# Performance work log

Hardware: AMD Instinct MI355X
Metric: run time of the kernel (lower is better)

The kernel has to match this reference:

```python
import jax, jax.numpy as jnp
import numpy as np

HEADS, DIM_HEAD = 16, 64
MAX_FREQ = 256.0

def axial_freqs(H, W):
    # rotary_embedding_torch, freqs_for='pixel': base freqs = linspace(1, max_freq/2, dim//2)*pi
    # with rotary dim = DIM_HEAD//2 per axis, so DIM_HEAD//4 base frequencies per axis.
    nf = DIM_HEAD // 4
    base = jnp.linspace(1.0, MAX_FREQ / 2.0, nf) * jnp.pi
    def per_axis(n):
        pos = jnp.linspace(-1.0, 1.0, n)              # pixel positions in [-1, 1]
        fr = pos[:, None] * base[None, :]             # (n, DIM_HEAD//4)
        return jnp.repeat(fr, 2, axis=-1)             # (n, DIM_HEAD//2), interleaved repeat
    fh = jnp.broadcast_to(per_axis(H)[:, None, :], (H, W, DIM_HEAD // 2))
    fw = jnp.broadcast_to(per_axis(W)[None, :, :], (H, W, DIM_HEAD // 2))
    return jnp.concatenate([fh, fw], axis=-1)         # (H, W, DIM_HEAD)

def rotate_half(x):
    # interleaved-pair rotation: (x0,x1,x2,x3,...) -> (-x1,x0,-x3,x2,...)
    x2 = x.reshape(x.shape[:-1] + (-1, 2))
    a, b = x2[..., 0], x2[..., 1]
    return jnp.stack([-b, a], axis=-1).reshape(x.shape)

def apply_rot(freqs, t):
    return t * jnp.cos(freqs) + rotate_half(t) * jnp.sin(freqs)

def setup_inputs() -> dict:
    key = jax.random.key(0)
    ks = jax.random.split(key, 6)
    B, T, H, W, dim = 1, 2, 16, 16, 1024
    inner = HEADS * DIM_HEAD
    S, K = H * W, 144
    x = jax.random.normal(ks[0], (B, T, H, W, dim), jnp.float32)
    w_qkv = jax.random.normal(ks[1], (3 * inner, dim), jnp.float32) * (dim ** -0.5)
    w_out = jax.random.normal(ks[2], (dim, inner), jnp.float32) * (inner ** -0.5)
    b_out = jnp.zeros((dim,), jnp.float32)
    out_not_top_k = jax.random.normal(ks[3], (B * T, HEADS, S, DIM_HEAD), jnp.float32) * 0.02
    top_k_indices = jax.random.randint(ks[4], (B * T, HEADS, S, K), 0, S, jnp.int32)
    return {"x": x, "w_qkv": w_qkv, "w_out": w_out, "b_out": b_out,
            "out_not_top_k": out_not_top_k, "top_k_indices": top_k_indices}

def reference(x, w_qkv, w_out, b_out, out_not_top_k, top_k_indices):
    B, T, H, W, dim = x.shape
    inner = HEADS * DIM_HEAD
    S = H * W
    # qkv projection (torch Linear: y = x @ W^T)
    qkv = jnp.einsum('bthwc,oc->bthwo', x, w_qkv)
    q, k, v = jnp.split(qkv, 3, axis=-1)

    def to_grid(t):
        t = t.reshape(B * T, H, W, HEADS, DIM_HEAD)
        return jnp.transpose(t, (0, 3, 1, 2, 4))       # (BT, h, H, W, d)
    q, k, v = map(to_grid, (q, k, v))

    freqs = axial_freqs(H, W)                          # (H, W, d), broadcasts over (BT, h)
    q = apply_rot(freqs, q)
    k = apply_rot(freqs, k)

    q = q.reshape(B * T, HEADS, S, DIM_HEAD)
    k = k.reshape(B * T, HEADS, S, DIM_HEAD)
    v = v.reshape(B * T, HEADS, S, DIM_HEAD)

    scale = DIM_HEAD ** -0.5
    idx = top_k_indices[..., None]                      # (BT, h, S, K, 1)
    # per-query gather of top-k keys/values: out[b,h,s,k,:] = k[b,h,idx[b,h,s,k],:]
    k_g = jnp.take_along_axis(k[:, :, None, :, :], idx, axis=3)  # (BT, h, S, K, d)
    v_g = jnp.take_along_axis(v[:, :, None, :, :], idx, axis=3)

    scores = jnp.einsum('bhsd,bhskd->bhsk', q, k_g) * scale
    probs = jax.nn.softmax(scores, axis=-1)
    out_top = jnp.einsum('bhsk,bhskd->bhsd', probs, v_g)

    out = out_top + out_not_top_k                       # (BT, h, S, d)
    out = jnp.transpose(out.reshape(B * T, HEADS, H, W, DIM_HEAD), (0, 2, 3, 1, 4))
    out = out.reshape(B, T, H, W, inner)
    return jnp.einsum('bthwi,oi->bthwo', out, w_out) + b_out
```

## Files before the change

### kernel.cpp

```cpp
#include <hip/hip_runtime.h>
#include <hip/hip_bf16.h>
#include <math.h>

#define BTN   2
#define NH    16
#define SEQ   256
#define DH    64
#define DIMF  1024
#define KTOP  144
#define QT    32
#define PI_F  3.14159265358979323846f

typedef _Float16 half8 __attribute__((ext_vector_type(8)));
typedef _Float16 half4v __attribute__((ext_vector_type(4)));
typedef float f32x4 __attribute__((ext_vector_type(4)));

#define GLDS(src, dst) __builtin_amdgcn_global_load_lds( \
        (const __attribute__((address_space(1))) void*)(src), \
        (__attribute__((address_space(3))) void*)(dst), 16, 0, 0)

#define N0Q (524288 / 4)
#define N1Q (3145728 / 4)
#define N2Q (1048576 / 4)
__global__ __launch_bounds__(256)
void cvt3_kernel(const float* __restrict__ a, const float* __restrict__ b,
                 const float* __restrict__ c,
                 _Float16* __restrict__ da, _Float16* __restrict__ db,
                 _Float16* __restrict__ dc)
{
    int q = blockIdx.x * 256 + threadIdx.x;
    const float* s; _Float16* d; int off;
    if (q < N0Q)            { s = a; d = da; off = q; }
    else if (q < N0Q + N1Q) { s = b; d = db; off = q - N0Q; }
    else                    { s = c; d = dc; off = q - (N0Q + N1Q); }
    const float4 v = *(const float4*)(s + (size_t)off * 4);
    half4v h;
    h[0] = (_Float16)v.x; h[1] = (_Float16)v.y;
    h[2] = (_Float16)v.z; h[3] = (_Float16)v.w;
    *(half4v*)(d + (size_t)off * 4) = h;
}

template <int MODE, int Kd>
__global__ __launch_bounds__(256)
void gemm_f16_kernel(const _Float16* __restrict__ A, const _Float16* __restrict__ B,
                     int N,
                     _Float16* __restrict__ qb, _Float16* __restrict__ kb,
                     _Float16* __restrict__ vb,
                     const float* __restrict__ bias, float* __restrict__ out)
{
    __shared__ __align__(16) _Float16 As[64 * 64];
    __shared__ __align__(16) _Float16 Bs[64 * 64];

    const int tid  = threadIdx.x;
    const int wave = tid >> 6;
    const int lane = tid & 63;
    const int row0 = blockIdx.y * 64;
    const int col0 = blockIdx.x * 64;
    const int wr = (wave >> 1) * 32;
    const int wc = (wave & 1) * 32;
    const int rl = lane >> 3;
    const int cl = lane & 7;

    f32x4 acc[2][2] = {};

    for (int kt = 0; kt < Kd; kt += 64) {
        __syncthreads();
#pragma unroll
        for (int h = 0; h < 2; ++h) {
            const int rbase = wave * 16 + h * 8;
            const int rA = rbase + rl;
            const _Float16* srcA = A + (size_t)(row0 + rA) * Kd + kt + ((cl ^ (rA & 7)) * 8);
            const _Float16* srcB = B + (size_t)(col0 + rA) * Kd + kt + ((cl ^ (rA & 7)) * 8);
            GLDS(srcA, As + rbase * 64);
            GLDS(srcB, Bs + rbase * 64);
        }
        __syncthreads();

#pragma unroll
        for (int kh = 0; kh < 2; ++kh) {
            half8 a[2], b[2];
            const int g = kh * 4 + (lane >> 4);
#pragma unroll
            for (int i = 0; i < 2; ++i) {
                const int ra = wr + i * 16 + (lane & 15);
                const int rb = wc + i * 16 + (lane & 15);
                a[i] = *(const half8*)(As + ra * 64 + ((g ^ (ra & 7)) * 8));
                b[i] = *(const half8*)(Bs + rb * 64 + ((g ^ (rb & 7)) * 8));
            }
#pragma unroll
            for (int i = 0; i < 2; ++i)
#pragma unroll
                for (int j = 0; j < 2; ++j)
                    acc[i][j] = __builtin_amdgcn_mfma_f32_16x16x32_f16(a[i], b[j], acc[i][j], 0, 0, 0);
        }
    }

    if (MODE == 0) {
#pragma unroll
        for (int i = 0; i < 2; ++i) {
#pragma unroll
            for (int reg = 0; reg < 4; ++reg) {
                const int r  = row0 + wr + i * 16 + (lane >> 4) * 4 + reg;
                const int bt = r >> 8;
                const int s  = r & 255;
                const int hh = s >> 4;
                const int ww = s & 15;
#pragma unroll
                for (int j = 0; j < 2; ++j) {
                    const float v     = acc[i][j][reg];
                    const float other = __shfl_xor(v, 1);
                    const int n    = col0 + wc + j * 16 + (lane & 15);
                    const int sec  = n >> 10;
                    const int oi   = n & 1023;
                    const int head = oi >> 6;
                    const int d    = oi & 63;
                    if (sec == 2) {
                        vb[(((size_t)(bt * NH + head)) * DH + d) * SEQ + s] = (_Float16)v;
                    } else {
                        const int de  = d & ~1;
                        const int j2  = (de < 32) ? (de >> 1) : ((de - 32) >> 1);
                        const float pos = (de < 32) ? (-1.f + hh * (2.f / 15.f))
                                                    : (-1.f + ww * (2.f / 15.f));
                        const float f  = pos * (PI_F * (1.f + j2 * (127.f / 15.f)));
                        const float cf = __cosf(f), sf = __sinf(f);
                        const float res = (d & 1) ? (v * cf + other * sf)
                                                  : (v * cf - other * sf);
                        _Float16* dp = (sec == 0) ? qb : kb;
                        dp[(((size_t)(bt * NH + head)) * SEQ + s) * DH + d] = (_Float16)res;
                    }
                }
            }
        }
    } else {
#pragma unroll
        for (int i = 0; i < 2; ++i)
#pragma unroll
            for (int reg = 0; reg < 4; ++reg) {
                const int r = row0 + wr + i * 16 + (lane >> 4) * 4 + reg;
#pragma unroll
                for (int j = 0; j < 2; ++j) {
                    const int n = col0 + wc + j * 16 + (lane & 15);
                    out[(size_t)r * N + n] = acc[i][j][reg] + bias[n];
                }
            }
    }
}

__global__ __launch_bounds__(512)
void attn_dense_kernel(const _Float16* __restrict__ qh, const _Float16* __restrict__ kh,
                       const _Float16* __restrict__ vt, const int* __restrict__ topk,
                       const float* __restrict__ ontk, _Float16* __restrict__ attnh)
{
    __shared__ __align__(16) _Float16 Qs[QT * DH];
    __shared__ __align__(16) _Float16 Ks[SEQ * DH];
    __shared__ __align__(16) _Float16 VTs[DH * SEQ];
    __shared__ __align__(16) float    Ps[QT * 260];

    const int tid  = threadIdx.x;
    const int w    = tid >> 6;
    const int lane = tid & 63;
    const int bid  = blockIdx.x;
    const int bt   = bid >> 7;
    const int head = (bid >> 3) & 15;
    const int s0   = (bid & 7) * QT;

    const _Float16* kbase  = kh + ((size_t)(bt * NH + head)) * SEQ * DH;
    const _Float16* vtbase = vt + ((size_t)(bt * NH + head)) * DH * SEQ;
    const _Float16* qbase  = qh + (((size_t)(bt * NH + head)) * SEQ + s0) * DH;

#pragma unroll
    for (int h = 0; h < 4; ++h) {
        const int r = w * 32 + h * 8 + (lane >> 3);
        GLDS(kbase + (size_t)r * DH + (((lane & 7) ^ (r & 7)) * 8), Ks + (w * 32 + h * 8) * DH);
    }
#pragma unroll
    for (int h = 0; h < 4; ++h) {
        const int r = w * 8 + h * 2 + (lane >> 5);
        GLDS(vtbase + (size_t)r * SEQ + (((lane & 31) ^ (r & 7)) * 8), VTs + (w * 8 + h * 2) * SEQ);
    }
    if (w < 4) {
        const int r = w * 8 + (lane >> 3);
        GLDS(qbase + (size_t)r * DH + (((lane & 7) ^ (r & 7)) * 8), Qs + (w * 8) * DH);
    }
    __syncthreads();

    f32x4 acc[2][2] = {};
#pragma unroll
    for (int kk = 0; kk < 2; ++kk) {
        half8 a[2], b[2];
        const int c = kk * 4 + (lane >> 4);
#pragma unroll
        for (int i = 0; i < 2; ++i) {
            const int ra = i * 16 + (lane & 15);
            const int rb = w * 32 + i * 16 + (lane & 15);
            a[i] = *(const half8*)(Qs + ra * DH + ((c ^ (ra & 7)) * 8));
            b[i] = *(const half8*)(Ks + rb * DH + ((c ^ (rb & 7)) * 8));
        }
#pragma unroll
        for (int i = 0; i < 2; ++i)
#pragma unroll
            for (int j = 0; j < 2; ++j)
                acc[i][j] = __builtin_amdgcn_mfma_f32_16x16x32_f16(a[i], b[j], acc[i][j], 0, 0, 0);
    }
#pragma unroll
    for (int i = 0; i < 2; ++i)
#pragma unroll
        for (int j = 0; j < 2; ++j)
#pragma unroll
            for (int reg = 0; reg < 4; ++reg) {
                const int row = i * 16 + (lane >> 4) * 4 + reg;
                const int col = w * 32 + j * 16 + (lane & 15);
                Ps[row * 260 + col] = acc[i][j][reg];
            }
    __syncthreads();

#pragma unroll
    for (int qq = 0; qq < 4; ++qq) {
        const int q = w * 4 + qq;
        const size_t gq = ((size_t)(bt * NH + head)) * SEQ + s0 + q;
        const int* idxp = topk + gq * KTOP;
        const int ki0 = idxp[lane];
        const int ki1 = idxp[lane + 64];
        const int ki2 = (lane < 16) ? idxp[lane + 128] : 0;
        const float sv0 = Ps[q * 260 + ki0] * 0.125f;
        const float sv1 = Ps[q * 260 + ki1] * 0.125f;
        const float sv2 = (lane < 16) ? Ps[q * 260 + ki2] * 0.125f : -1e30f;
        float m = fmaxf(fmaxf(sv0, sv1), sv2);
#pragma unroll
        for (int off = 32; off; off >>= 1) m = fmaxf(m, __shfl_xor(m, off));
        const float e0 = __expf(sv0 - m);
        const float e1 = __expf(sv1 - m);
        const float e2 = (lane < 16) ? __expf(sv2 - m) : 0.f;
        float z = e0 + e1 + e2;
#pragma unroll
        for (int off = 32; off; off >>= 1) z += __shfl_xor(z, off);
        const float inv = 1.f / z;
        for (int c2 = lane; c2 < 260; c2 += 64) Ps[q * 260 + c2] = 0.f;
        atomicAdd(&Ps[q * 260 + ki0], e0 * inv);
        atomicAdd(&Ps[q * 260 + ki1], e1 * inv);
        if (lane < 16) atomicAdd(&Ps[q * 260 + ki2], e2 * inv);
    }
    __syncthreads();

    const int iw = w >> 2;
    const int jw = w & 3;
    f32x4 oacc = {};
#pragma unroll
    for (int ks = 0; ks < 8; ++ks) {
        const int ra = iw * 16 + (lane & 15);
        const float* pp = Ps + ra * 260 + ks * 32 + (lane >> 4) * 8;
        const float4 p0 = *(const float4*)pp;
        const float4 p1 = *(const float4*)(pp + 4);
        half8 af;
        af[0] = (_Float16)p0.x; af[1] = (_Float16)p0.y;
        af[2] = (_Float16)p0.z; af[3] = (_Float16)p0.w;
        af[4] = (_Float16)p1.x; af[5] = (_Float16)p1.y;
        af[6] = (_Float16)p1.z; af[7] = (_Float16)p1.w;
        const int d = jw * 16 + (lane & 15);
        const int c = ks * 4 + (lane >> 4);
        const half8 bf = *(const half8*)(VTs + d * SEQ + ((c ^ (d & 7)) * 8));
        oacc = __builtin_amdgcn_mfma_f32_16x16x32_f16(af, bf, oacc, 0, 0, 0);
    }
#pragma unroll
    for (int reg = 0; reg < 4; ++reg) {
        const int row = iw * 16 + (lane >> 4) * 4 + reg;
        const int d   = jw * 16 + (lane & 15);
        const int s   = s0 + row;
        const float v = oacc[reg] +
            ontk[(((size_t)(bt * NH + head)) * SEQ + s) * DH + d];
        attnh[((size_t)(bt * SEQ + s)) * DIMF + head * DH + d] = (_Float16)v;
    }
}

extern "C" void kernel_launch(void* const* d_in, const int* in_sizes, int n_in,
                              void* d_out, int out_size, void* d_ws, size_t ws_size,
                              hipStream_t stream) {
    const float* x     = (const float*)d_in[0];
    const float* w_qkv = (const float*)d_in[1];
    const float* w_out = (const float*)d_in[2];
    const float* b_out = (const float*)d_in[3];
    const float* ontk  = (const float*)d_in[4];
    const int*   topk  = (const int*)d_in[5];
    float* out = (float*)d_out;

    const size_t QE = (size_t)BTN * NH * SEQ * DH;

    _Float16* xh    = (_Float16*)d_ws;
    _Float16* wqh   = xh + 524288;
    _Float16* woh   = wqh + 3145728;
    _Float16* attnh = woh + 1048576;
    _Float16* qhb   = attnh + QE;
    _Float16* khb   = qhb + QE;
    _Float16* vtb   = khb + QE;

    cvt3_kernel<<<(N0Q + N1Q + N2Q) / 256, 256, 0, stream>>>(x, w_qkv, w_out, xh, wqh, woh);

    gemm_f16_kernel<0, DIMF><<<dim3(3072 / 64, 512 / 64), 256, 0, stream>>>(
        xh, wqh, 3072, qhb, khb, vtb, nullptr, nullptr);

    attn_dense_kernel<<<BTN * NH * (SEQ / QT), 512, 0, stream>>>(
        qhb, khb, vtb, topk, ontk, attnh);

    gemm_f16_kernel<1, DIMF><<<dim3(1024 / 64, 512 / 64), 256, 0, stream>>>(
        attnh, woh, 1024, nullptr, nullptr, nullptr, b_out, out);
}
```

Before: 50.49 us.

## Fuse fp32-to-fp16 conversion into GEMM tile loads with register prefetch

Removes the separate conversion kernel that cast x, w_qkv and w_out to fp16. The GEMMs now read fp32 directly, convert in registers and store swizzled fp16 tiles to LDS. The next tile is prefetched into registers while MFMA runs on the current one. This saves a launch and a full write plus re-read of the converted weights, but each GEMM block now re-reads and re-converts fp32 data, which doubles the global bytes for those operands.

```diff
diff --git a/kernel.cpp b/kernel.cpp
--- a/kernel.cpp
+++ b/kernel.cpp
@@ -19,31 +19,14 @@
         (const __attribute__((address_space(1))) void*)(src), \
         (__attribute__((address_space(3))) void*)(dst), 16, 0, 0)
 
-#define N0Q (524288 / 4)
-#define N1Q (3145728 / 4)
-#define N2Q (1048576 / 4)
-__global__ __launch_bounds__(256)
-void cvt3_kernel(const float* __restrict__ a, const float* __restrict__ b,
-                 const float* __restrict__ c,
-                 _Float16* __restrict__ da, _Float16* __restrict__ db,
-                 _Float16* __restrict__ dc)
-{
-    int q = blockIdx.x * 256 + threadIdx.x;
-    const float* s; _Float16* d; int off;
-    if (q < N0Q)            { s = a; d = da; off = q; }
-    else if (q < N0Q + N1Q) { s = b; d = db; off = q - N0Q; }
-    else                    { s = c; d = dc; off = q - (N0Q + N1Q); }
-    const float4 v = *(const float4*)(s + (size_t)off * 4);
-    half4v h;
-    h[0] = (_Float16)v.x; h[1] = (_Float16)v.y;
-    h[2] = (_Float16)v.z; h[3] = (_Float16)v.w;
-    *(half4v*)(d + (size_t)off * 4) = h;
+__device__ __forceinline__ int swz_b(int r, int c) {
+    return r * 128 + (((c >> 3) ^ (r & 7)) * 16) + ((c >> 2) & 1) * 8;
 }
 
 template <int MODE, int Kd>
-__global__ __launch_bounds__(256)
-void gemm_f16_kernel(const _Float16* __restrict__ A, const _Float16* __restrict__ B,
-                     int N,
+__global__ __launch_bounds__(256, 2)
+void gemm_f16_kernel(const float* __restrict__ A32, const _Float16* __restrict__ A16,
+                     const float* __restrict__ B32, int N,
                      _Float16* __restrict__ qb, _Float16* __restrict__ kb,
                      _Float16* __restrict__ vb,
                      const float* __restrict__ bias, float* __restrict__ out)
@@ -58,23 +41,65 @@
     const int col0 = blockIdx.x * 64;
     const int wr = (wave >> 1) * 32;
     const int wc = (wave & 1) * 32;
-    const int rl = lane >> 3;
-    const int cl = lane & 7;
+
+    const int sr = tid >> 4;
+    const int sc = (tid & 15) * 4;
+
+    float4 areg[4], breg[4];
+    const int NT = Kd / 64;
+
+    if (MODE == 0) {
+#pragma unroll
+        for (int p = 0; p < 4; ++p)
+            areg[p] = *(const float4*)(A32 + (size_t)(row0 + p * 16 + sr) * Kd + sc);
+    }
+#pragma unroll
+    for (int p = 0; p < 4; ++p)
+        breg[p] = *(const float4*)(B32 + (size_t)(col0 + p * 16 + sr) * Kd + sc);
 
     f32x4 acc[2][2] = {};
 
-    for (int kt = 0; kt < Kd; kt += 64) {
+    for (int kt = 0; kt < NT; ++kt) {
         __syncthreads();
-#pragma unroll
-        for (int h = 0; h < 2; ++h) {
-            const int rbase = wave * 16 + h * 8;
-            const int rA = rbase + rl;
-            const _Float16* srcA = A + (size_t)(row0 + rA) * Kd + kt + ((cl ^ (rA & 7)) * 8);
-            const _Float16* srcB = B + (size_t)(col0 + rA) * Kd + kt + ((cl ^ (rA & 7)) * 8);
-            GLDS(srcA, As + rbase * 64);
-            GLDS(srcB, Bs + rbase * 64);
+        if (MODE == 0) {
+#pragma unroll
+            for (int p = 0; p < 4; ++p) {
+                const int r = p * 16 + sr;
+                half4v h;
+                h[0] = (_Float16)areg[p].x; h[1] = (_Float16)areg[p].y;
+                h[2] = (_Float16)areg[p].z; h[3] = (_Float16)areg[p].w;
+                *(half4v*)((char*)As + swz_b(r, sc)) = h;
+            }
+        } else {
+#pragma unroll
+            for (int h = 0; h < 2; ++h) {
+                const int rbase = wave * 16 + h * 8;
+                const int rA = rbase + (lane >> 3);
+                GLDS(A16 + (size_t)(row0 + rA) * Kd + kt * 64 + (((lane & 7) ^ (rA & 7)) * 8),
+                     As + rbase * 64);
+            }
+        }
+#pragma unroll
+        for (int p = 0; p < 4; ++p) {
+            const int r = p * 16 + sr;
+            half4v h;
+            h[0] = (_Float16)breg[p].x; h[1] = (_Float16)breg[p].y;
+            h[2] = (_Float16)breg[p].z; h[3] = (_Float16)breg[p].w;
+            *(half4v*)((char*)Bs + swz_b(r, sc)) = h;
         }
         __syncthreads();
+
+        if (kt + 1 < NT) {
+            const int kn = (kt + 1) * 64;
+            if (MODE == 0) {
+#pragma unroll
+                for (int p = 0; p < 4; ++p)
+                    areg[p] = *(const float4*)(A32 + (size_t)(row0 + p * 16 + sr) * Kd + kn + sc);
+            }
+#pragma unroll
+            for (int p = 0; p < 4; ++p)
+                breg[p] = *(const float4*)(B32 + (size_t)(col0 + p * 16 + sr) * Kd + kn + sc);
+        }
 
 #pragma unroll
         for (int kh = 0; kh < 2; ++kh) {
@@ -84,8 +109,8 @@
             for (int i = 0; i < 2; ++i) {
                 const int ra = wr + i * 16 + (lane & 15);
                 const int rb = wc + i * 16 + (lane & 15);
-                a[i] = *(const half8*)(As + ra * 64 + ((g ^ (ra & 7)) * 8));
-                b[i] = *(const half8*)(Bs + rb * 64 + ((g ^ (rb & 7)) * 8));
+                a[i] = *(const half8*)((char*)As + ra * 128 + ((g ^ (ra & 7)) * 16));
+                b[i] = *(const half8*)((char*)Bs + rb * 128 + ((g ^ (rb & 7)) * 16));
             }
 #pragma unroll
             for (int i = 0; i < 2; ++i)
@@ -285,22 +310,17 @@
 
     const size_t QE = (size_t)BTN * NH * SEQ * DH;
 
-    _Float16* xh    = (_Float16*)d_ws;
-    _Float16* wqh   = xh + 524288;
-    _Float16* woh   = wqh + 3145728;
-    _Float16* attnh = woh + 1048576;
-    _Float16* qhb   = attnh + QE;
+    _Float16* attnh = (_Float16*)d_ws;
+    _Float16* qhb   = attnh + (size_t)512 * 1024;
     _Float16* khb   = qhb + QE;
     _Float16* vtb   = khb + QE;
 
-    cvt3_kernel<<<(N0Q + N1Q + N2Q) / 256, 256, 0, stream>>>(x, w_qkv, w_out, xh, wqh, woh);
-
     gemm_f16_kernel<0, DIMF><<<dim3(3072 / 64, 512 / 64), 256, 0, stream>>>(
-        xh, wqh, 3072, qhb, khb, vtb, nullptr, nullptr);
+        x, nullptr, w_qkv, 3072, qhb, khb, vtb, nullptr, nullptr);
 
     attn_dense_kernel<<<BTN * NH * (SEQ / QT), 512, 0, stream>>>(
         qhb, khb, vtb, topk, ontk, attnh);
 
     gemm_f16_kernel<1, DIMF><<<dim3(1024 / 64, 512 / 64), 256, 0, stream>>>(
-        attnh, woh, 1024, nullptr, nullptr, nullptr, b_out, out);
+        nullptr, attnh, w_out, 1024, nullptr, nullptr, nullptr, b_out, out);
 }
```

Measured after the change: 61.62 us. 1.22x slower.

## Load Q/K/V fragments straight into registers and drop LDS staging in attention

Applied to the files above, without the earlier changes.

The attention kernel no longer stages full K, V^T and Q tiles in shared memory. Each wave loads its MFMA fragments directly from global memory into registers, and the top-k indices and out_not_top_k values are fetched up front so their latency overlaps. The score buffer switches from row padding to an XOR swizzle, which cuts shared memory to about 32KB per block and should allow more blocks per CU. The cost is more register pressure and redundant global reads of K and V across waves, which now rely on L2.

```diff
diff --git a/kernel.cpp b/kernel.cpp
--- a/kernel.cpp
+++ b/kernel.cpp
@@ -147,14 +147,11 @@
 }
 
 __global__ __launch_bounds__(512)
-void attn_dense_kernel(const _Float16* __restrict__ qh, const _Float16* __restrict__ kh,
-                       const _Float16* __restrict__ vt, const int* __restrict__ topk,
-                       const float* __restrict__ ontk, _Float16* __restrict__ attnh)
+void attn_reg_kernel(const _Float16* __restrict__ qh, const _Float16* __restrict__ kh,
+                     const _Float16* __restrict__ vt, const int* __restrict__ topk,
+                     const float* __restrict__ ontk, _Float16* __restrict__ attnh)
 {
-    __shared__ __align__(16) _Float16 Qs[QT * DH];
-    __shared__ __align__(16) _Float16 Ks[SEQ * DH];
-    __shared__ __align__(16) _Float16 VTs[DH * SEQ];
-    __shared__ __align__(16) float    Ps[QT * 260];
+    __shared__ __align__(16) float Ps[QT * 256];
 
     const int tid  = threadIdx.x;
     const int w    = tid >> 6;
@@ -163,45 +160,51 @@
     const int bt   = bid >> 7;
     const int head = (bid >> 3) & 15;
     const int s0   = (bid & 7) * QT;
-
-    const _Float16* kbase  = kh + ((size_t)(bt * NH + head)) * SEQ * DH;
-    const _Float16* vtbase = vt + ((size_t)(bt * NH + head)) * DH * SEQ;
-    const _Float16* qbase  = qh + (((size_t)(bt * NH + head)) * SEQ + s0) * DH;
-
-#pragma unroll
-    for (int h = 0; h < 4; ++h) {
-        const int r = w * 32 + h * 8 + (lane >> 3);
-        GLDS(kbase + (size_t)r * DH + (((lane & 7) ^ (r & 7)) * 8), Ks + (w * 32 + h * 8) * DH);
-    }
-#pragma unroll
-    for (int h = 0; h < 4; ++h) {
-        const int r = w * 8 + h * 2 + (lane >> 5);
-        GLDS(vtbase + (size_t)r * SEQ + (((lane & 31) ^ (r & 7)) * 8), VTs + (w * 8 + h * 2) * SEQ);
-    }
-    if (w < 4) {
-        const int r = w * 8 + (lane >> 3);
-        GLDS(qbase + (size_t)r * DH + (((lane & 7) ^ (r & 7)) * 8), Qs + (w * 8) * DH);
-    }
-    __syncthreads();
+    const int bh   = bt * NH + head;
+    const int iw   = w >> 2;
+    const int jw   = w & 3;
+
+    int ki0[4], ki1[4], ki2[4];
+#pragma unroll
+    for (int qq = 0; qq < 4; ++qq) {
+        const int* idxp = topk + ((size_t)bh * SEQ + s0 + w * 4 + qq) * KTOP;
+        ki0[qq] = idxp[lane];
+        ki1[qq] = idxp[lane + 64];
+        ki2[qq] = idxp[(lane < 16) ? (lane + 128) : lane];
+    }
+    float on[4];
+#pragma unroll
+    for (int reg = 0; reg < 4; ++reg) {
+        const int row = iw * 16 + (lane >> 4) * 4 + reg;
+        on[reg] = ontk[((size_t)bh * SEQ + s0 + row) * DH + jw * 16 + (lane & 15)];
+    }
+    half8 bv[8];
+    {
+        const _Float16* vrow = vt + ((size_t)bh * DH + jw * 16 + (lane & 15)) * SEQ
+                                  + (lane >> 4) * 8;
+#pragma unroll
+        for (int ks = 0; ks < 8; ++ks)
+            bv[ks] = *(const half8*)(vrow + ks * 32);
+    }
+    half8 aq[2][2], bk[2][2];
+#pragma unroll
+    for (int kk = 0; kk < 2; ++kk) {
+        const int c8 = (kk * 4 + (lane >> 4)) * 8;
+#pragma unroll
+        for (int i = 0; i < 2; ++i) {
+            aq[kk][i] = *(const half8*)(qh + ((size_t)bh * SEQ + s0 + i * 16 + (lane & 15)) * DH + c8);
+            bk[kk][i] = *(const half8*)(kh + ((size_t)bh * SEQ + w * 32 + i * 16 + (lane & 15)) * DH + c8);
+        }
+    }
 
     f32x4 acc[2][2] = {};
 #pragma unroll
-    for (int kk = 0; kk < 2; ++kk) {
-        half8 a[2], b[2];
-        const int c = kk * 4 + (lane >> 4);
-#pragma unroll
-        for (int i = 0; i < 2; ++i) {
-            const int ra = i * 16 + (lane & 15);
-            const int rb = w * 32 + i * 16 + (lane & 15);
-            a[i] = *(const half8*)(Qs + ra * DH + ((c ^ (ra & 7)) * 8));
-            b[i] = *(const half8*)(Ks + rb * DH + ((c ^ (rb & 7)) * 8));
-        }
+    for (int kk = 0; kk < 2; ++kk)
 #pragma unroll
         for (int i = 0; i < 2; ++i)
 #pragma unroll
             for (int j = 0; j < 2; ++j)
-                acc[i][j] = __builtin_amdgcn_mfma_f32_16x16x32_f16(a[i], b[j], acc[i][j], 0, 0, 0);
-    }
+                acc[i][j] = __builtin_amdgcn_mfma_f32_16x16x32_f16(aq[kk][i], bk[kk][j], acc[i][j], 0, 0, 0);
 #pragma unroll
     for (int i = 0; i < 2; ++i)
 #pragma unroll
@@ -210,21 +213,18 @@
             for (int reg = 0; reg < 4; ++reg) {
                 const int row = i * 16 + (lane >> 4) * 4 + reg;
                 const int col = w * 32 + j * 16 + (lane & 15);
-                Ps[row * 260 + col] = acc[i][j][reg];
+                Ps[row * 256 + (col ^ ((row & 7) << 2))] = acc[i][j][reg];
             }
     __syncthreads();
 
 #pragma unroll
     for (int qq = 0; qq < 4; ++qq) {
-        const int q = w * 4 + qq;
-        const size_t gq = ((size_t)(bt * NH + head)) * SEQ + s0 + q;
-        const int* idxp = topk + gq * KTOP;
-        const int ki0 = idxp[lane];
-        const int ki1 = idxp[lane + 64];
-        const int ki2 = (lane < 16) ? idxp[lane + 128] : 0;
-        const float sv0 = Ps[q * 260 + ki0] * 0.125f;
-        const float sv1 = Ps[q * 260 + ki1] * 0.125f;
-        const float sv2 = (lane < 16) ? Ps[q * 260 + ki2] * 0.125f : -1e30f;
+        const int q  = w * 4 + qq;
+        const int sw = (q & 7) << 2;
+        float* prow  = Ps + q * 256;
+        const float sv0 = prow[ki0[qq] ^ sw] * 0.125f;
+        const float sv1 = prow[ki1[qq] ^ sw] * 0.125f;
+        const float sv2 = (lane < 16) ? prow[ki2[qq] ^ sw] * 0.125f : -1e30f;
         float m = fmaxf(fmaxf(sv0, sv1), sv2);
 #pragma unroll
         for (int off = 32; off; off >>= 1) m = fmaxf(m, __shfl_xor(m, off));
@@ -235,40 +235,35 @@
 #pragma unroll
         for (int off = 32; off; off >>= 1) z += __shfl_xor(z, off);
         const float inv = 1.f / z;
-        for (int c2 = lane; c2 < 260; c2 += 64) Ps[q * 260 + c2] = 0.f;
-        atomicAdd(&Ps[q * 260 + ki0], e0 * inv);
-        atomicAdd(&Ps[q * 260 + ki1], e1 * inv);
-        if (lane < 16) atomicAdd(&Ps[q * 260 + ki2], e2 * inv);
+#pragma unroll
+        for (int c2 = 0; c2 < 4; ++c2) prow[lane + c2 * 64] = 0.f;
+        atomicAdd(&prow[ki0[qq] ^ sw], e0 * inv);
+        atomicAdd(&prow[ki1[qq] ^ sw], e1 * inv);
+        if (lane < 16) atomicAdd(&prow[ki2[qq] ^ sw], e2 * inv);
     }
     __syncthreads();
 
-    const int iw = w >> 2;
-    const int jw = w & 3;
     f32x4 oacc = {};
 #pragma unroll
     for (int ks = 0; ks < 8; ++ks) {
         const int ra = iw * 16 + (lane & 15);
-        const float* pp = Ps + ra * 260 + ks * 32 + (lane >> 4) * 8;
-        const float4 p0 = *(const float4*)pp;
-        const float4 p1 = *(const float4*)(pp + 4);
+        const int b0 = ks * 32 + (lane >> 4) * 8;
+        const int sw = (ra & 7) << 2;
+        const float4 p0 = *(const float4*)(Ps + ra * 256 + (b0 ^ sw));
+        const float4 p1 = *(const float4*)(Ps + ra * 256 + ((b0 + 4) ^ sw));
         half8 af;
         af[0] = (_Float16)p0.x; af[1] = (_Float16)p0.y;
         af[2] = (_Float16)p0.z; af[3] = (_Float16)p0.w;
         af[4] = (_Float16)p1.x; af[5] = (_Float16)p1.y;
         af[6] = (_Float16)p1.z; af[7] = (_Float16)p1.w;
-        const int d = jw * 16 + (lane & 15);
-        const int c = ks * 4 + (lane >> 4);
-        const half8 bf = *(const half8*)(VTs + d * SEQ + ((c ^ (d & 7)) * 8));
-        oacc = __builtin_amdgcn_mfma_f32_16x16x32_f16(af, bf, oacc, 0, 0, 0);
+        oacc = __builtin_amdgcn_mfma_f32_16x16x32_f16(af, bv[ks], oacc, 0, 0, 0);
     }
 #pragma unroll
     for (int reg = 0; reg < 4; ++reg) {
         const int row = iw * 16 + (lane >> 4) * 4 + reg;
         const int d   = jw * 16 + (lane & 15);
         const int s   = s0 + row;
-        const float v = oacc[reg] +
-            ontk[(((size_t)(bt * NH + head)) * SEQ + s) * DH + d];
-        attnh[((size_t)(bt * SEQ + s)) * DIMF + head * DH + d] = (_Float16)v;
+        attnh[((size_t)(bt * SEQ + s)) * DIMF + head * DH + d] = (_Float16)(oacc[reg] + on[reg]);
     }
 }
 
@@ -298,7 +293,7 @@
     gemm_f16_kernel<0, DIMF><<<dim3(3072 / 64, 512 / 64), 256, 0, stream>>>(
         xh, wqh, 3072, qhb, khb, vtb, nullptr, nullptr);
 
-    attn_dense_kernel<<<BTN * NH * (SEQ / QT), 512, 0, stream>>>(
+    attn_reg_kernel<<<BTN * NH * (SEQ / QT), 512, 0, stream>>>(
         qhb, khb, vtb, topk, ontk, attnh);
 
     gemm_f16_kernel<1, DIMF><<<dim3(1024 / 64, 512 / 64), 256, 0, stream>>>(
```

New measurement: 49.61 us. About the same (-1.8%).
